# Kernel tuning notes

Hardware: AMD Instinct MI355X
Metric: run time of the kernel (lower is better)

Reference implementation:

```python
import jax, jax.numpy as jnp
import numpy as np

B, T, V, E, H, LAT, L = 2048, 120, 64, 128, 512, 256, 2


def setup_inputs() -> dict:
    key = jax.random.key(0)
    ks = jax.random.split(key, 16)
    s = 0.05  # weight init scale
    z = jax.random.normal(ks[0], (B, LAT), jnp.float32)
    target = jax.random.randint(ks[1], (B, T), 0, V)
    embed = (jax.random.normal(ks[2], (V, E), jnp.float32) * s).at[0].set(0.0)  # padding_idx=0
    fc_hidden_w = jax.random.normal(ks[3], (H * L, LAT), jnp.float32) * s
    fc_hidden_b = jax.random.normal(ks[4], (H * L,), jnp.float32) * s
    W_ih0 = jax.random.normal(ks[5], (3 * H, E + LAT), jnp.float32) * s
    W_hh0 = jax.random.normal(ks[6], (3 * H, H), jnp.float32) * s
    b_ih0 = jax.random.normal(ks[7], (3 * H,), jnp.float32) * s
    b_hh0 = jax.random.normal(ks[8], (3 * H,), jnp.float32) * s
    W_ih1 = jax.random.normal(ks[9], (3 * H, H), jnp.float32) * s
    W_hh1 = jax.random.normal(ks[10], (3 * H, H), jnp.float32) * s
    b_ih1 = jax.random.normal(ks[11], (3 * H,), jnp.float32) * s
    b_hh1 = jax.random.normal(ks[12], (3 * H,), jnp.float32) * s
    fc_out_w = jax.random.normal(ks[13], (V, H), jnp.float32) * s
    fc_out_b = jax.random.normal(ks[14], (V,), jnp.float32) * s
    return dict(z=z, target=target, embed=embed, fc_hidden_w=fc_hidden_w,
                fc_hidden_b=fc_hidden_b, W_ih0=W_ih0, W_hh0=W_hh0, b_ih0=b_ih0,
                b_hh0=b_hh0, W_ih1=W_ih1, W_hh1=W_hh1, b_ih1=b_ih1, b_hh1=b_hh1,
                fc_out_w=fc_out_w, fc_out_b=fc_out_b)


def _gru_cell(x, h, W_ih, W_hh, b_ih, b_hh):
    # torch GRU cell: r,z,n gate ordering
    gx = x @ W_ih.T + b_ih          # [B, 3H]
    gh = h @ W_hh.T + b_hh          # [B, 3H]
    xr, xz, xn = jnp.split(gx, 3, axis=-1)
    hr, hz, hn = jnp.split(gh, 3, axis=-1)
    r = jax.nn.sigmoid(xr + hr)
    u = jax.nn.sigmoid(xz + hz)
    n = jnp.tanh(xn + r * hn)
    return (1.0 - u) * n + u * h


def reference(z, target, embed, fc_hidden_w, fc_hidden_b, W_ih0, W_hh0, b_ih0,
              b_hh0, W_ih1, W_hh1, b_ih1, b_hh1, fc_out_w, fc_out_b):
    b, lat = z.shape
    t = target.shape[1]
    hd = W_hh0.shape[1]
    # initial hidden: fc_hidden(z).view(B, L, H) -> per-layer states
    hid = (z @ fc_hidden_w.T + fc_hidden_b).reshape(b, L, hd)
    h0, h1 = hid[:, 0, :], hid[:, 1, :]
    # teacher forcing with ratio 1.0: input_0 = token 1, input_t = target[:, t-1]
    tok = jnp.concatenate([jnp.ones((b, 1), target.dtype), target[:, :-1]], axis=1)
    # precompute per-step GRU inputs: [T, B, E+LAT]
    xs = jnp.concatenate(
        [embed[tok], jnp.broadcast_to(z[:, None, :], (b, t, lat))], axis=-1)
    xs = jnp.swapaxes(xs, 0, 1)

    def step(carry, x):
        h0, h1 = carry
        h0n = _gru_cell(x, h0, W_ih0, W_hh0, b_ih0, b_hh0)
        h1n = _gru_cell(h0n, h1, W_ih1, W_hh1, b_ih1, b_hh1)
        logits = h1n @ fc_out_w.T + fc_out_b
        return (h0n, h1n), logits

    _, out = jax.lax.scan(step, (h0, h1), xs)   # [T, B, V]
    return jnp.swapaxes(out, 0, 1)              # [B, T, V]
```

## Files before the change

kernel.cpp:

```cpp
#include <hip/hip_runtime.h>
#include <hip/hip_bf16.h>

#define DI __device__ __forceinline__

typedef short bf16x8 __attribute__((ext_vector_type(8)));
typedef float f32x4 __attribute__((ext_vector_type(4)));

constexpr int B_ = 2048, T_ = 120, V_ = 64, E_ = 128, H_ = 512, LAT_ = 256;
constexpr int H3 = 1536;

DI short f2b(float f) {
  union { __hip_bfloat16 h; short s; } u;
  u.h = __float2bfloat16(f);
  return u.s;
}
DI float b2f(short s) {
  union { unsigned u; float f; } x;
  x.u = (unsigned)(unsigned short)s << 16;
  return x.f;
}
DI float sigm(float x) { return 1.f / (1.f + __expf(-x)); }
DI float tanh_f(float x) {
  x = fminf(15.f, fmaxf(-15.f, x));
  float e = __expf(2.f * x);
  return (e - 1.f) / (e + 1.f);
}
DI float gru_one(float xr, float xz, float xn, float hr, float hz, float hn, float hp) {
  float r = sigm(xr + hr);
  float u = sigm(xz + hz);
  float nn = tanh_f(xn + r * hn);
  return (1.f - u) * nn + u * hp;
}
DI float gru_pre(float sr, float sz, float xn, float hn, float hp) {
  float r = sigm(sr);
  float u = sigm(sz);
  float nn = tanh_f(xn + r * hn);
  return (1.f - u) * nn + u * hp;
}

template <int ROWS, int BK, int NV>
DI void rs_load(const short* __restrict__ G, int row0, int K, int kk, bf16x8 (&v)[NV]) {
  constexpr int SLOTS = BK / 8;
  constexpr int RPP = 2048 / BK;
  static_assert(NV == ROWS / RPP, "NV mismatch");
  const int tid = threadIdx.x;
  const int rl = tid / SLOTS, sl = tid % SLOTS;
#pragma unroll
  for (int p = 0; p < NV; ++p)
    v[p] = *(const bf16x8*)(G + (size_t)(row0 + p * RPP + rl) * K + kk + sl * 8);
}
template <int ROWS, int BK, int NV>
DI void rs_write(char* __restrict__ lds, bf16x8 (&v)[NV]) {
  constexpr int SLOTS = BK / 8;
  constexpr int RPP = 2048 / BK;
  const int tid = threadIdx.x;
  const int rl = tid / SLOTS, sl = tid % SLOTS;
#pragma unroll
  for (int p = 0; p < NV; ++p) {
    int row = p * RPP + rl;
    *(bf16x8*)(lds + row * (SLOTS * 16) + ((sl ^ (row & (SLOTS - 1))) * 16)) = v[p];
  }
}
template <int BK>
DI bf16x8 fragL(const char* __restrict__ lds, int row, int kk) {
  return *(const bf16x8*)(lds + row * (BK * 2) + ((kk << 1) ^ ((row & (BK / 8 - 1)) << 4)));
}

DI void gemm_core(const short* __restrict__ A, const short* __restrict__ Bw,
                  int arow, int bcol, char* lds, f32x4 (&acc)[2][4]) {
  char* As[2] = {lds, lds + 8192};
  char* Bs[2] = {lds + 16384, lds + 32768};
  const int tid = threadIdx.x, lane = tid & 63, wid = tid >> 6;
  const int wm = wid >> 1, wn = wid & 1;
  const int r = lane & 15, ko = (lane >> 4) * 8;
  bf16x8 va[2], vb[4];
  rs_load<64, 64, 2>(A, arow, H_, 0, va);
  rs_load<128, 64, 4>(Bw, bcol, H_, 0, vb);
  rs_write<64, 64, 2>(As[0], va);
  rs_write<128, 64, 4>(Bs[0], vb);
  __syncthreads();
  int cur = 0;
  for (int c = 0; c < 8; ++c) {
    if (c < 7) {
      rs_load<64, 64, 2>(A, arow, H_, (c + 1) * 64, va);
      rs_load<128, 64, 4>(Bw, bcol, H_, (c + 1) * 64, vb);
    }
#pragma unroll
    for (int kh = 0; kh < 2; ++kh) {
      const int kkk = kh * 32 + ko;
      bf16x8 a[2], b[4];
#pragma unroll
      for (int i = 0; i < 2; ++i) a[i] = fragL<64>(As[cur], wm * 32 + i * 16 + r, kkk);
#pragma unroll
      for (int j = 0; j < 4; ++j) b[j] = fragL<64>(Bs[cur], wn * 64 + j * 16 + r, kkk);
#pragma unroll
      for (int i = 0; i < 2; ++i)
#pragma unroll
        for (int j = 0; j < 4; ++j)
          acc[i][j] = __builtin_amdgcn_mfma_f32_16x16x32_bf16(a[i], b[j], acc[i][j], 0, 0, 0);
    }
    if (c < 7) {
      rs_write<64, 64, 2>(As[cur ^ 1], va);
      rs_write<128, 64, 4>(Bs[cur ^ 1], vb);
    }
    __syncthreads();
    cur ^= 1;
  }
}

struct GArgs {
  const short* zgx; const short* egx; const int* target;
  float* h0f; float* h1f; short* h0b; short* h1b;
  short* p0;
  short* gx1; short* gh1;
  const short* Wb_hh0; const float* b_hh0;
  const short* Wb_ih1; const float* b_ih1;
  const short* Wb_hh1; const float* b_hh1;
  const short* Wb_out; const float* fc_out_b;
  float* out;
};

__global__ __launch_bounds__(256) void k_L1(GArgs a, int t) {
  extern __shared__ char smem[];
  const int u = blockIdx.x;
  const int tid = threadIdx.x, lane = tid & 63, wid = tid >> 6;
  const int wm = wid >> 1, wn = wid & 1;
  const int r0 = (lane >> 4) * 4, c0 = lane & 15;
  if (u < 768) {
    const int grp = u / 24;
    const int rem = u % 24;
    const int nt = rem % 12;
    const int arow = grp * 64, bcol = nt * 128;
    if (rem < 12) {
      if (t >= T_) return;
      f32x4 acc[2][4] = {};
      gemm_core(a.h0b, a.Wb_hh0, arow, bcol, smem, acc);
      const int g = nt >> 2;
#pragma unroll
      for (int i = 0; i < 2; ++i)
#pragma unroll
        for (int j = 0; j < 4; ++j) {
          const int col = bcol + wn * 64 + j * 16 + c0;
          const int jj = col & 511;
          const float bv = a.b_hh0[col];
#pragma unroll
          for (int rr = 0; rr < 4; ++rr) {
            const int row = arow + wm * 32 + i * 16 + r0 + rr;
            const float val = acc[i][j][rr] + bv;
            const int tok = (t == 0) ? 1 : a.target[(size_t)row * T_ + (t - 1)];
            const float xv = b2f(a.zgx[(size_t)row * H3 + g * 512 + jj]) +
                             b2f(a.egx[(size_t)tok * H3 + g * 512 + jj]);
            short* pr = a.p0 + ((size_t)row * 4) * 512 + jj;
            if (g < 2) {
              pr[g * 512] = f2b(val + xv);
            } else {
              pr[2 * 512] = f2b(xv);
              pr[3 * 512] = f2b(val);
            }
          }
        }
    } else {
      if (t < 1) return;
      f32x4 acc[2][4] = {};
      gemm_core(a.h0b, a.Wb_ih1, arow, bcol, smem, acc);
#pragma unroll
      for (int i = 0; i < 2; ++i)
#pragma unroll
        for (int j = 0; j < 4; ++j) {
          const int col = bcol + wn * 64 + j * 16 + c0;
          const float bv = a.b_ih1[col];
#pragma unroll
          for (int rr = 0; rr < 4; ++rr)
            a.gx1[(size_t)(arow + wm * 32 + i * 16 + r0 + rr) * H3 + col] =
                f2b(acc[i][j][rr] + bv);
        }
    }
    return;
  }
  if (t < 1) return;
  const int uu = u - 768;
  const int mt = uu / 12, nt = uu % 12;
  const int arow = mt * 64, bcol = nt * 128;
  f32x4 acc[2][4] = {};
  gemm_core(a.h1b, a.Wb_hh1, arow, bcol, smem, acc);
#pragma unroll
  for (int i = 0; i < 2; ++i)
#pragma unroll
    for (int j = 0; j < 4; ++j) {
      const int col = bcol + wn * 64 + j * 16 + c0;
      const float bv = a.b_hh1[col];
#pragma unroll
      for (int rr = 0; rr < 4; ++rr)
        a.gh1[(size_t)(arow + wm * 32 + i * 16 + r0 + rr) * H3 + col] =
            f2b(acc[i][j][rr] + bv);
    }
}

__global__ __launch_bounds__(256) void k_L2(GArgs a, int t) {
  extern __shared__ char smem[];
  const int u = blockIdx.x;
  const int tid = threadIdx.x;
  if (u < 128) {
    if (t >= T_) return;
    const int row0 = u * 16;
#pragma unroll 1
    for (int it = 0; it < 4; ++it) {
      int v = it * 256 + tid;
      int rl = v >> 6, jb = v & 63;
      int row = row0 + rl, j = jb * 8;
      const short* pr = a.p0 + ((size_t)row * 4) * 512 + j;
      bf16x8 sr = *(const bf16x8*)(pr);
      bf16x8 sz = *(const bf16x8*)(pr + 512);
      bf16x8 xn = *(const bf16x8*)(pr + 1024);
      bf16x8 hn = *(const bf16x8*)(pr + 1536);
      float* hf = a.h0f + (size_t)row * H_ + j;
      float4 hp0 = *(const float4*)(hf);
      float4 hp1 = *(const float4*)(hf + 4);
      float hp[8] = {hp0.x, hp0.y, hp0.z, hp0.w, hp1.x, hp1.y, hp1.z, hp1.w};
      float hv[8];
      bf16x8 ov;
#pragma unroll
      for (int e = 0; e < 8; ++e) {
        hv[e] = gru_pre(b2f(sr[e]), b2f(sz[e]), b2f(xn[e]), b2f(hn[e]), hp[e]);
        ov[e] = f2b(hv[e]);
      }
      *(float4*)(hf) = make_float4(hv[0], hv[1], hv[2], hv[3]);
      *(float4*)(hf + 4) = make_float4(hv[4], hv[5], hv[6], hv[7]);
      *(bf16x8*)(a.h0b + (size_t)row * H_ + j) = ov;
    }
    return;
  }
  if (t < 1) return;
  short* sh = (short*)smem;
  const int row0 = (u - 128) * 16;
  const int tlog = t - 1;
#pragma unroll 1
  for (int c = 0; c < 4; ++c) {
    int f = c * 2048 + tid * 8;
    int rl = f >> 9, j = f & 511;
    int row = row0 + rl;
    const short* gx = a.gx1 + (size_t)row * H3 + j;
    const short* gh = a.gh1 + (size_t)row * H3 + j;
    float* hf = a.h1f + (size_t)row * H_ + j;
    bf16x8 xr = *(const bf16x8*)(gx);
    bf16x8 xz = *(const bf16x8*)(gx + H_);
    bf16x8 xn = *(const bf16x8*)(gx + 2 * H_);
    bf16x8 hr = *(const bf16x8*)(gh);
    bf16x8 hz = *(const bf16x8*)(gh + H_);
    bf16x8 hn = *(const bf16x8*)(gh + 2 * H_);
    float4 hp0 = *(const float4*)(hf);
    float4 hp1 = *(const float4*)(hf + 4);
    float hp[8] = {hp0.x, hp0.y, hp0.z, hp0.w, hp1.x, hp1.y, hp1.z, hp1.w};
    float hv[8];
    bf16x8 ov;
#pragma unroll
    for (int e = 0; e < 8; ++e) {
      hv[e] = gru_one(b2f(xr[e]), b2f(xz[e]), b2f(xn[e]),
                      b2f(hr[e]), b2f(hz[e]), b2f(hn[e]), hp[e]);
      ov[e] = f2b(hv[e]);
    }
    *(float4*)(hf) = make_float4(hv[0], hv[1], hv[2], hv[3]);
    *(float4*)(hf + 4) = make_float4(hv[4], hv[5], hv[6], hv[7]);
    *(bf16x8*)(a.h1b + (size_t)row * H_ + j) = ov;
    *(bf16x8*)(&sh[rl * 520 + j]) = ov;
  }
  __syncthreads();
  const int lane = tid & 63, w = tid >> 6;
  const int c0 = lane & 15, ko = (lane >> 4) * 8;
  f32x4 acc = {};
  const short* wb = a.Wb_out + (size_t)(w * 16 + c0) * H_ + ko;
  const short* ap = &sh[c0 * 520 + ko];
#pragma unroll
  for (int m = 0; m < 16; ++m) {
    bf16x8 av = *(const bf16x8*)(ap + m * 32);
    bf16x8 bw = *(const bf16x8*)(wb + m * 32);
    acc = __builtin_amdgcn_mfma_f32_16x16x32_bf16(av, bw, acc, 0, 0, 0);
  }
  const int r0 = (lane >> 4) * 4;
  const int col = w * 16 + c0;
  const float bv = a.fc_out_b[col];
#pragma unroll
  for (int rr = 0; rr < 4; ++rr) {
    int brow = row0 + r0 + rr;
    a.out[((size_t)brow * T_ + tlog) * V_ + col] = acc[rr] + bv;
  }
}

template <int MI, int NJ>
DI void gemm_wave_global(const short* __restrict__ A, const short* __restrict__ B,
                         const int K, const int arow, const int bcol,
                         f32x4 (&acc)[MI][NJ]) {
  const int lane = threadIdx.x & 63;
  const int r = lane & 15, ko = (lane >> 4) * 8;
  const short* Ap = A + (size_t)(arow + r) * K + ko;
  const short* Bp = B + (size_t)(bcol + r) * K + ko;
  for (int kk = 0; kk < K; kk += 32) {
    bf16x8 a[MI], b[NJ];
#pragma unroll
    for (int i = 0; i < MI; ++i) a[i] = *(const bf16x8*)(Ap + (size_t)i * 16 * K + kk);
#pragma unroll
    for (int j = 0; j < NJ; ++j) b[j] = *(const bf16x8*)(Bp + (size_t)j * 16 * K + kk);
#pragma unroll
    for (int i = 0; i < MI; ++i)
#pragma unroll
      for (int j = 0; j < NJ; ++j)
        acc[i][j] = __builtin_amdgcn_mfma_f32_16x16x32_bf16(a[i], b[j], acc[i][j], 0, 0, 0);
  }
}
template <int MI, int NJ>
DI void epi_store_bf16(short* __restrict__ C, const float* __restrict__ bias,
                       const int N, const int arow, const int bcol, f32x4 (&acc)[MI][NJ]) {
  const int lane = threadIdx.x & 63;
  const int r0 = (lane >> 4) * 4, c0 = lane & 15;
#pragma unroll
  for (int i = 0; i < MI; ++i)
#pragma unroll
    for (int j = 0; j < NJ; ++j) {
      int col = bcol + j * 16 + c0;
      float bv = bias[col];
#pragma unroll
      for (int rr = 0; rr < 4; ++rr)
        C[(size_t)(arow + i * 16 + r0 + rr) * N + col] = f2b(acc[i][j][rr] + bv);
    }
}

__global__ __launch_bounds__(256) void k_prep0(
    const float* __restrict__ W_hh0, const float* __restrict__ W_ih1,
    const float* __restrict__ W_hh1, const float* __restrict__ fc_out_w,
    const float* __restrict__ W_ih0, const float* __restrict__ fc_hidden_w,
    const float* __restrict__ z,
    short* Wb_hh0, short* Wb_ih1, short* Wb_hh1, short* Wb_out,
    short* Wb_ih0z, short* Wb_fch, short* z_b) {
  const int n1 = H3 * H_;
  const int n2 = V_ * H_;
  const int n3 = H3 * LAT_;
  const int n4 = (2 * H_) * LAT_;
  const int n5 = B_ * LAT_;
  const int total = n1 * 3 + n2 + n3 + n4 + n5;
  for (int i = blockIdx.x * blockDim.x + threadIdx.x; i < total;
       i += gridDim.x * blockDim.x) {
    int idx = i;
    if (idx < n1) { Wb_hh0[idx] = f2b(W_hh0[idx]); continue; }
    idx -= n1;
    if (idx < n1) { Wb_ih1[idx] = f2b(W_ih1[idx]); continue; }
    idx -= n1;
    if (idx < n1) { Wb_hh1[idx] = f2b(W_hh1[idx]); continue; }
    idx -= n1;
    if (idx < n2) { Wb_out[idx] = f2b(fc_out_w[idx]); continue; }
    idx -= n2;
    if (idx < n3) {
      int n = idx >> 8, k = idx & 255;
      Wb_ih0z[idx] = f2b(W_ih0[(size_t)n * (E_ + LAT_) + E_ + k]);
      continue;
    }
    idx -= n3;
    if (idx < n4) { Wb_fch[idx] = f2b(fc_hidden_w[idx]); continue; }
    idx -= n4;
    z_b[idx] = f2b(z[idx]);
  }
}

__global__ __launch_bounds__(256) void k_prep_emb(const float* __restrict__ embed,
                                                  const float* __restrict__ W_ih0,
                                                  short* __restrict__ egx) {
  __shared__ float er[E_];
  int v = blockIdx.x;
  for (int e = threadIdx.x; e < E_; e += blockDim.x) er[e] = embed[(size_t)v * E_ + e];
  __syncthreads();
  for (int n = threadIdx.x; n < H3; n += blockDim.x) {
    const float* w = W_ih0 + (size_t)n * (E_ + LAT_);
    float acc = 0.f;
#pragma unroll 8
    for (int e = 0; e < E_; ++e) acc += er[e] * w[e];
    egx[(size_t)v * H3 + n] = f2b(acc);
  }
}

__global__ __launch_bounds__(256) void k_prep1(
    const short* __restrict__ z_b, const short* __restrict__ Wb_ih0z,
    const short* __restrict__ Wb_fch, const float* __restrict__ b_ih0,
    const float* __restrict__ fc_hidden_b,
    short* zgx, float* h0f, float* h1f, short* h0b, short* h1b) {
  const int bid = blockIdx.x;
  const int mtile = bid / 20, ntile = bid % 20;
  const int tid = threadIdx.x, lane = tid & 63, wid = tid >> 6;
  const int wm = wid >> 1, wn = wid & 1;
  const int arow = mtile * 128 + wm * 64;
  f32x4 acc[4][4] = {};
  if (ntile < 12) {
    int bcol = ntile * 128 + wn * 64;
    gemm_wave_global<4, 4>(z_b, Wb_ih0z, LAT_, arow, bcol, acc);
    epi_store_bf16<4, 4>(zgx, b_ih0, H3, arow, bcol, acc);
  } else {
    int bcol = (ntile - 12) * 128 + wn * 64;
    gemm_wave_global<4, 4>(z_b, Wb_fch, LAT_, arow, bcol, acc);
    const int r0 = (lane >> 4) * 4, c0 = lane & 15;
#pragma unroll
    for (int i = 0; i < 4; ++i)
#pragma unroll
      for (int j = 0; j < 4; ++j) {
        int col = bcol + j * 16 + c0;
        float bv = fc_hidden_b[col];
#pragma unroll
        for (int rr = 0; rr < 4; ++rr) {
          int row = arow + i * 16 + r0 + rr;
          float v = acc[i][j][rr] + bv;
          if (col < H_) {
            h0f[(size_t)row * H_ + col] = v;
            h0b[(size_t)row * H_ + col] = f2b(v);
          } else {
            h1f[(size_t)row * H_ + (col - H_)] = v;
            h1b[(size_t)row * H_ + (col - H_)] = f2b(v);
          }
        }
      }
  }
}

extern "C" void kernel_launch(void* const* d_in, const int* in_sizes, int n_in,
                              void* d_out, int out_size, void* d_ws, size_t ws_size,
                              hipStream_t stream) {
  const float* z           = (const float*)d_in[0];
  const int*   target      = (const int*)d_in[1];
  const float* embed       = (const float*)d_in[2];
  const float* fc_hidden_w = (const float*)d_in[3];
  const float* fc_hidden_b = (const float*)d_in[4];
  const float* W_ih0       = (const float*)d_in[5];
  const float* W_hh0       = (const float*)d_in[6];
  const float* b_ih0       = (const float*)d_in[7];
  const float* b_hh0       = (const float*)d_in[8];
  const float* W_ih1       = (const float*)d_in[9];
  const float* W_hh1       = (const float*)d_in[10];
  const float* b_ih1       = (const float*)d_in[11];
  const float* b_hh1       = (const float*)d_in[12];
  const float* fc_out_w    = (const float*)d_in[13];
  const float* fc_out_b    = (const float*)d_in[14];
  float* out = (float*)d_out;

  char* ws = (char*)d_ws;
  size_t off = 0;
  auto alloc = [&](size_t bytes) -> void* {
    off = (off + 255) & ~(size_t)255;
    void* p = ws + off;
    off += bytes;
    return p;
  };
  float* h0f    = (float*)alloc((size_t)B_ * H_ * 4);
  float* h1f    = (float*)alloc((size_t)B_ * H_ * 4);
  short* h0b    = (short*)alloc((size_t)B_ * H_ * 2);
  short* h1b    = (short*)alloc((size_t)B_ * H_ * 2);
  short* p0     = (short*)alloc((size_t)B_ * 4 * H_ * 2);
  short* gx1    = (short*)alloc((size_t)B_ * H3 * 2);
  short* gh1    = (short*)alloc((size_t)B_ * H3 * 2);
  short* zgx    = (short*)alloc((size_t)B_ * H3 * 2);
  short* egx    = (short*)alloc((size_t)V_ * H3 * 2);
  short* Wb_hh0 = (short*)alloc((size_t)H3 * H_ * 2);
  short* Wb_ih1 = (short*)alloc((size_t)H3 * H_ * 2);
  short* Wb_hh1 = (short*)alloc((size_t)H3 * H_ * 2);
  short* Wb_out = (short*)alloc((size_t)V_ * H_ * 2);
  short* Wb_ih0z= (short*)alloc((size_t)H3 * LAT_ * 2);
  short* Wb_fch = (short*)alloc((size_t)2 * H_ * LAT_ * 2);
  short* z_b    = (short*)alloc((size_t)B_ * LAT_ * 2);
  if (off > ws_size) return;

  k_prep0<<<2048, 256, 0, stream>>>(W_hh0, W_ih1, W_hh1, fc_out_w, W_ih0, fc_hidden_w,
                                    z, Wb_hh0, Wb_ih1, Wb_hh1, Wb_out, Wb_ih0z, Wb_fch, z_b);
  k_prep_emb<<<64, 256, 0, stream>>>(embed, W_ih0, egx);
  k_prep1<<<320, 256, 0, stream>>>(z_b, Wb_ih0z, Wb_fch, b_ih0, fc_hidden_b,
                                   zgx, h0f, h1f, h0b, h1b);

  GArgs a;
  a.zgx = zgx; a.egx = egx; a.target = target;
  a.h0f = h0f; a.h1f = h1f; a.h0b = h0b; a.h1b = h1b;
  a.p0 = p0; a.gx1 = gx1; a.gh1 = gh1;
  a.Wb_hh0 = Wb_hh0; a.b_hh0 = b_hh0;
  a.Wb_ih1 = Wb_ih1; a.b_ih1 = b_ih1;
  a.Wb_hh1 = Wb_hh1; a.b_hh1 = b_hh1;
  a.Wb_out = Wb_out; a.fc_out_b = fc_out_b;
  a.out = out;

  for (int t = 0; t <= T_; ++t) {
    k_L1<<<1152, 256, 49152, stream>>>(a, t);
    k_L2<<<256, 256, 16640, stream>>>(a, t);
  }
}
```

Measured before the change: 4.647 ms.

## Use 128x128 GEMM tiles and move output projection into next step's L1 kernel

Replaces the 64x128 GEMM tile with a 128x128 tile (BK=32, 4x4 MFMA per wave) and cuts LDS to 32KB, allowing 3 blocks per CU. This raises arithmetic intensity per tile and occupancy. The fc_out projection moves out of k_L2 into a separate block range of k_L1, running one step later, which adds an extra launch iteration. k_L2 now handles 32 rows per block with fewer blocks and no LDS.

```diff
diff --git a/kernel.cpp b/kernel.cpp
--- a/kernel.cpp
+++ b/kernel.cpp
@@ -66,42 +66,38 @@
   return *(const bf16x8*)(lds + row * (BK * 2) + ((kk << 1) ^ ((row & (BK / 8 - 1)) << 4)));
 }
 
-DI void gemm_core(const short* __restrict__ A, const short* __restrict__ Bw,
-                  int arow, int bcol, char* lds, f32x4 (&acc)[2][4]) {
+DI void gemm128(const short* __restrict__ A, const short* __restrict__ Bw,
+                int arow, int bcol, char* lds, f32x4 (&acc)[4][4]) {
   char* As[2] = {lds, lds + 8192};
-  char* Bs[2] = {lds + 16384, lds + 32768};
+  char* Bs[2] = {lds + 16384, lds + 24576};
   const int tid = threadIdx.x, lane = tid & 63, wid = tid >> 6;
   const int wm = wid >> 1, wn = wid & 1;
   const int r = lane & 15, ko = (lane >> 4) * 8;
-  bf16x8 va[2], vb[4];
-  rs_load<64, 64, 2>(A, arow, H_, 0, va);
-  rs_load<128, 64, 4>(Bw, bcol, H_, 0, vb);
-  rs_write<64, 64, 2>(As[0], va);
-  rs_write<128, 64, 4>(Bs[0], vb);
+  bf16x8 va[2], vb[2];
+  rs_load<128, 32, 2>(A, arow, H_, 0, va);
+  rs_load<128, 32, 2>(Bw, bcol, H_, 0, vb);
+  rs_write<128, 32, 2>(As[0], va);
+  rs_write<128, 32, 2>(Bs[0], vb);
   __syncthreads();
   int cur = 0;
-  for (int c = 0; c < 8; ++c) {
-    if (c < 7) {
-      rs_load<64, 64, 2>(A, arow, H_, (c + 1) * 64, va);
-      rs_load<128, 64, 4>(Bw, bcol, H_, (c + 1) * 64, vb);
-    }
-#pragma unroll
-    for (int kh = 0; kh < 2; ++kh) {
-      const int kkk = kh * 32 + ko;
-      bf16x8 a[2], b[4];
-#pragma unroll
-      for (int i = 0; i < 2; ++i) a[i] = fragL<64>(As[cur], wm * 32 + i * 16 + r, kkk);
-#pragma unroll
-      for (int j = 0; j < 4; ++j) b[j] = fragL<64>(Bs[cur], wn * 64 + j * 16 + r, kkk);
-#pragma unroll
-      for (int i = 0; i < 2; ++i)
-#pragma unroll
-        for (int j = 0; j < 4; ++j)
-          acc[i][j] = __builtin_amdgcn_mfma_f32_16x16x32_bf16(a[i], b[j], acc[i][j], 0, 0, 0);
-    }
-    if (c < 7) {
-      rs_write<64, 64, 2>(As[cur ^ 1], va);
-      rs_write<128, 64, 4>(Bs[cur ^ 1], vb);
+  for (int c = 0; c < 16; ++c) {
+    if (c < 15) {
+      rs_load<128, 32, 2>(A, arow, H_, (c + 1) * 32, va);
+      rs_load<128, 32, 2>(Bw, bcol, H_, (c + 1) * 32, vb);
+    }
+    bf16x8 af[4], bf[4];
+#pragma unroll
+    for (int i = 0; i < 4; ++i) af[i] = fragL<32>(As[cur], wm * 64 + i * 16 + r, ko);
+#pragma unroll
+    for (int j = 0; j < 4; ++j) bf[j] = fragL<32>(Bs[cur], wn * 64 + j * 16 + r, ko);
+#pragma unroll
+    for (int i = 0; i < 4; ++i)
+#pragma unroll
+      for (int j = 0; j < 4; ++j)
+        acc[i][j] = __builtin_amdgcn_mfma_f32_16x16x32_bf16(af[i], bf[j], acc[i][j], 0, 0, 0);
+    if (c < 15) {
+      rs_write<128, 32, 2>(As[cur ^ 1], va);
+      rs_write<128, 32, 2>(Bs[cur ^ 1], vb);
     }
     __syncthreads();
     cur ^= 1;
@@ -120,24 +116,23 @@
   float* out;
 };
 
-__global__ __launch_bounds__(256) void k_L1(GArgs a, int t) {
+__global__ __launch_bounds__(256, 3) void k_L1(GArgs a, int t) {
   extern __shared__ char smem[];
   const int u = blockIdx.x;
   const int tid = threadIdx.x, lane = tid & 63, wid = tid >> 6;
   const int wm = wid >> 1, wn = wid & 1;
-  const int r0 = (lane >> 4) * 4, c0 = lane & 15;
-  if (u < 768) {
-    const int grp = u / 24;
-    const int rem = u % 24;
-    const int nt = rem % 12;
-    const int arow = grp * 64, bcol = nt * 128;
+  const int r0 = (lane >> 4) * 4, c0 = lane & 15, ko = (lane >> 4) * 8;
+  if (u < 576) {
+    const int grp = u / 36, rem = u % 36;
+    const int arow = grp * 128;
     if (rem < 12) {
       if (t >= T_) return;
-      f32x4 acc[2][4] = {};
-      gemm_core(a.h0b, a.Wb_hh0, arow, bcol, smem, acc);
-      const int g = nt >> 2;
-#pragma unroll
-      for (int i = 0; i < 2; ++i)
+      const int bcol = rem * 128;
+      f32x4 acc[4][4] = {};
+      gemm128(a.h0b, a.Wb_hh0, arow, bcol, smem, acc);
+      const int g = rem >> 2;
+#pragma unroll
+      for (int i = 0; i < 4; ++i)
 #pragma unroll
         for (int j = 0; j < 4; ++j) {
           const int col = bcol + wn * 64 + j * 16 + c0;
@@ -145,7 +140,7 @@
           const float bv = a.b_hh0[col];
 #pragma unroll
           for (int rr = 0; rr < 4; ++rr) {
-            const int row = arow + wm * 32 + i * 16 + r0 + rr;
+            const int row = arow + wm * 64 + i * 16 + r0 + rr;
             const float val = acc[i][j][rr] + bv;
             const int tok = (t == 0) ? 1 : a.target[(size_t)row * T_ + (t - 1)];
             const float xv = b2f(a.zgx[(size_t)row * H3 + g * 512 + jj]) +
@@ -159,52 +154,68 @@
             }
           }
         }
-    } else {
-      if (t < 1) return;
-      f32x4 acc[2][4] = {};
-      gemm_core(a.h0b, a.Wb_ih1, arow, bcol, smem, acc);
-#pragma unroll
-      for (int i = 0; i < 2; ++i)
+    } else if (rem < 24) {
+      if (t < 1 || t > T_) return;
+      const int bcol = (rem - 12) * 128;
+      f32x4 acc[4][4] = {};
+      gemm128(a.h0b, a.Wb_ih1, arow, bcol, smem, acc);
+#pragma unroll
+      for (int i = 0; i < 4; ++i)
 #pragma unroll
         for (int j = 0; j < 4; ++j) {
           const int col = bcol + wn * 64 + j * 16 + c0;
           const float bv = a.b_ih1[col];
 #pragma unroll
           for (int rr = 0; rr < 4; ++rr)
-            a.gx1[(size_t)(arow + wm * 32 + i * 16 + r0 + rr) * H3 + col] =
+            a.gx1[(size_t)(arow + wm * 64 + i * 16 + r0 + rr) * H3 + col] =
                 f2b(acc[i][j][rr] + bv);
         }
+    } else {
+      if (t < 1 || t > T_) return;
+      const int bcol = (rem - 24) * 128;
+      f32x4 acc[4][4] = {};
+      gemm128(a.h1b, a.Wb_hh1, arow, bcol, smem, acc);
+#pragma unroll
+      for (int i = 0; i < 4; ++i)
+#pragma unroll
+        for (int j = 0; j < 4; ++j) {
+          const int col = bcol + wn * 64 + j * 16 + c0;
+          const float bv = a.b_hh1[col];
+#pragma unroll
+          for (int rr = 0; rr < 4; ++rr)
+            a.gh1[(size_t)(arow + wm * 64 + i * 16 + r0 + rr) * H3 + col] =
+                f2b(acc[i][j][rr] + bv);
+        }
     }
     return;
   }
-  if (t < 1) return;
-  const int uu = u - 768;
-  const int mt = uu / 12, nt = uu % 12;
-  const int arow = mt * 64, bcol = nt * 128;
-  f32x4 acc[2][4] = {};
-  gemm_core(a.h1b, a.Wb_hh1, arow, bcol, smem, acc);
-#pragma unroll
-  for (int i = 0; i < 2; ++i)
-#pragma unroll
-    for (int j = 0; j < 4; ++j) {
-      const int col = bcol + wn * 64 + j * 16 + c0;
-      const float bv = a.b_hh1[col];
-#pragma unroll
-      for (int rr = 0; rr < 4; ++rr)
-        a.gh1[(size_t)(arow + wm * 32 + i * 16 + r0 + rr) * H3 + col] =
-            f2b(acc[i][j][rr] + bv);
-    }
+  if (t < 2) return;
+  const int row0 = (u - 576) * 16;
+  const int tlog = t - 2;
+  const int w = wid;
+  f32x4 acc = {};
+  const short* ap = a.h1b + (size_t)(row0 + c0) * H_ + ko;
+  const short* wp = a.Wb_out + (size_t)(w * 16 + c0) * H_ + ko;
+#pragma unroll
+  for (int m = 0; m < 16; ++m) {
+    bf16x8 av = *(const bf16x8*)(ap + m * 32);
+    bf16x8 bw = *(const bf16x8*)(wp + m * 32);
+    acc = __builtin_amdgcn_mfma_f32_16x16x32_bf16(av, bw, acc, 0, 0, 0);
+  }
+  const float bv = a.fc_out_b[w * 16 + c0];
+#pragma unroll
+  for (int rr = 0; rr < 4; ++rr)
+    a.out[((size_t)(row0 + r0 + rr) * T_ + tlog) * V_ + w * 16 + c0] = acc[rr] + bv;
 }
 
 __global__ __launch_bounds__(256) void k_L2(GArgs a, int t) {
-  extern __shared__ char smem[];
   const int u = blockIdx.x;
   const int tid = threadIdx.x;
-  if (u < 128) {
+  if (u < 64) {
     if (t >= T_) return;
-    const int row0 = u * 16;
+    const int row0 = u * 32;
 #pragma unroll 1
-    for (int it = 0; it < 4; ++it) {
+    for (int it = 0; it < 8; ++it) {
       int v = it * 256 + tid;
       int rl = v >> 6, jb = v & 63;
       int row = row0 + rl, j = jb * 8;
@@ -230,15 +241,13 @@
     }
     return;
   }
-  if (t < 1) return;
-  short* sh = (short*)smem;
-  const int row0 = (u - 128) * 16;
-  const int tlog = t - 1;
+  if (t < 1 || t > T_) return;
+  const int row0 = (u - 64) * 32;
 #pragma unroll 1
-  for (int c = 0; c < 4; ++c) {
-    int f = c * 2048 + tid * 8;
-    int rl = f >> 9, j = f & 511;
-    int row = row0 + rl;
+  for (int it = 0; it < 8; ++it) {
+    int v = it * 256 + tid;
+    int rl = v >> 6, jb = v & 63;
+    int row = row0 + rl, j = jb * 8;
     const short* gx = a.gx1 + (size_t)row * H3 + j;
     const short* gh = a.gh1 + (size_t)row * H3 + j;
     float* hf = a.h1f + (size_t)row * H_ + j;
@@ -262,27 +271,6 @@
     *(float4*)(hf) = make_float4(hv[0], hv[1], hv[2], hv[3]);
     *(float4*)(hf + 4) = make_float4(hv[4], hv[5], hv[6], hv[7]);
     *(bf16x8*)(a.h1b + (size_t)row * H_ + j) = ov;
-    *(bf16x8*)(&sh[rl * 520 + j]) = ov;
-  }
-  __syncthreads();
-  const int lane = tid & 63, w = tid >> 6;
-  const int c0 = lane & 15, ko = (lane >> 4) * 8;
-  f32x4 acc = {};
-  const short* wb = a.Wb_out + (size_t)(w * 16 + c0) * H_ + ko;
-  const short* ap = &sh[c0 * 520 + ko];
-#pragma unroll
-  for (int m = 0; m < 16; ++m) {
-    bf16x8 av = *(const bf16x8*)(ap + m * 32);
-    bf16x8 bw = *(const bf16x8*)(wb + m * 32);
-    acc = __builtin_amdgcn_mfma_f32_16x16x32_bf16(av, bw, acc, 0, 0, 0);
-  }
-  const int r0 = (lane >> 4) * 4;
-  const int col = w * 16 + c0;
-  const float bv = a.fc_out_b[col];
-#pragma unroll
-  for (int rr = 0; rr < 4; ++rr) {
-    int brow = row0 + r0 + rr;
-    a.out[((size_t)brow * T_ + tlog) * V_ + col] = acc[rr] + bv;
   }
 }
 
@@ -479,8 +467,8 @@
   a.Wb_out = Wb_out; a.fc_out_b = fc_out_b;
   a.out = out;
 
-  for (int t = 0; t <= T_; ++t) {
-    k_L1<<<1152, 256, 49152, stream>>>(a, t);
-    k_L2<<<256, 256, 16640, stream>>>(a, t);
-  }
-}
+  for (int t = 0; t <= T_ + 1; ++t) {
+    k_L1<<<704, 256, 32768, stream>>>(a, t);
+    if (t <= T_) k_L2<<<128, 256, 0, stream>>>(a, t);
+  }
+}
```

New measurement: 7.550 ms. +62.4%, slower.
